# Kernel tuning notes

Measured on AMD Instinct MI355X. Metric: run time of the kernel, lower is better.

## Reference

```python
import jax, jax.numpy as jnp
import numpy as np

N_NODES = 100000
N_EDGES = 1600000
D_IN = 128
D_HID = 128
D_OUT = 128
N_LAYERS = 4


def setup_inputs() -> dict:
    key = jax.random.key(0)
    ks = jax.random.split(key, 8)
    x = jax.random.normal(ks[0], (N_NODES, D_IN), dtype=jnp.float32)
    edge_index = jax.random.randint(ks[1], (2, N_EDGES), 0, N_NODES, dtype=jnp.int64)
    s = 1.0 / np.sqrt(D_IN)
    # All layers are 128->128, so stack weights: [L, in, out]
    W_lin = jax.random.uniform(ks[2], (N_LAYERS, D_IN, D_HID), minval=-s, maxval=s, dtype=jnp.float32)
    W_film = jax.random.uniform(ks[3], (N_LAYERS, D_IN, 2 * D_HID), minval=-s, maxval=s, dtype=jnp.float32)
    b_film = jax.random.uniform(ks[4], (N_LAYERS, 2 * D_HID), minval=-s, maxval=s, dtype=jnp.float32)
    W_skip = jax.random.uniform(ks[5], (N_LAYERS, D_IN, D_HID), minval=-s, maxval=s, dtype=jnp.float32)
    W_fskip = jax.random.uniform(ks[6], (N_LAYERS, D_IN, 2 * D_HID), minval=-s, maxval=s, dtype=jnp.float32)
    return {"x": x, "edge_index": edge_index, "W_lin": W_lin, "W_film": W_film,
            "b_film": b_film, "W_skip": W_skip, "W_fskip": W_fskip}


def _film_conv(x, src, dst, deg_inv, W_l, W_f, b_f, W_s, W_fs, c):
    # skip path: FiLM-modulated self transform
    bg_s = x @ W_fs                       # [N, 2C], no bias
    beta_s, gamma_s = bg_s[:, :c], bg_s[:, c:]
    out = jax.nn.relu(gamma_s * (x @ W_s) + beta_s)
    # message path: FiLM params from target node, features from source node
    bg = x @ W_f + b_f                    # [N, 2C]
    beta, gamma = bg[:, :c], bg[:, c:]
    h = x @ W_l                           # [N, C]
    msg = jax.nn.relu(gamma[dst] * h[src] + beta[dst])  # [E, C]
    agg = jax.ops.segment_sum(msg, dst, num_segments=x.shape[0]) * deg_inv  # mean aggr
    return out + agg


def reference(x, edge_index, W_lin, W_film, b_film, W_skip, W_fskip):
    src, dst = edge_index[0], edge_index[1]
    n = x.shape[0]
    deg = jax.ops.segment_sum(jnp.ones((src.shape[0],), x.dtype), dst, num_segments=n)
    deg_inv = (1.0 / jnp.maximum(deg, 1.0))[:, None]   # clamp(min=1) like PyG mean
    for l in range(N_LAYERS):
        x = _film_conv(x, src, dst, deg_inv, W_lin[l], W_film[l], b_film[l],
                       W_skip[l], W_fskip[l], D_HID)
        if l < N_LAYERS - 1:
            x = jax.nn.relu(x)
    return x
```

## Files before the change

### kernel.cpp

```cpp
#include <hip/hip_runtime.h>
#include <hip/hip_bf16.h>

#define N_NODES 100000
#define N_PAD   100096
#define N_EDGES 1600000
#define NXCD    8
#define NRANGE  ((N_NODES + NXCD - 1) / NXCD)
#define NSLICE  256

typedef __bf16 bf16x8 __attribute__((ext_vector_type(8)));
typedef float  f32x4  __attribute__((ext_vector_type(4)));

__device__ __forceinline__ void gload16(const void* g, void* s) {
    __builtin_amdgcn_global_load_lds(
        (const __attribute__((address_space(1))) unsigned int*)g,
        (__attribute__((address_space(3))) unsigned int*)s, 16, 0, 0);
}

__device__ __forceinline__ float2 bf2f(unsigned p) {
    float2 r;
    union { unsigned u; float f; } a, b;
    a.u = p << 16;
    b.u = p & 0xffff0000u;
    r.x = a.f; r.y = b.f;
    return r;
}
__device__ __forceinline__ unsigned f2bf2(float x, float y) {
    unsigned lo = (unsigned)__builtin_bit_cast(unsigned short, __float2bfloat16(x));
    unsigned hi = (unsigned)__builtin_bit_cast(unsigned short, __float2bfloat16(y));
    return lo | (hi << 16);
}

__global__ void detect_kernel(const unsigned* __restrict__ e, int* __restrict__ flag) {
    __shared__ int nz;
    if (threadIdx.x == 0) nz = 0;
    __syncthreads();
    int local = 0;
    for (int i = threadIdx.x; i < 1024; i += blockDim.x)
        if (e[2 * i + 1] != 0) local = 1;
    if (local) atomicOr(&nz, 1);
    __syncthreads();
    if (threadIdx.x == 0) *flag = (nz == 0) ? 1 : 0;
}

__device__ __forceinline__ int edge_at(const unsigned* __restrict__ e, long idx, int is64) {
    return (int)(is64 ? e[2 * idx] : e[idx]);
}

__global__ void hist_kernel(const unsigned* __restrict__ e, const int* __restrict__ flag,
                            int* __restrict__ counts) {
    int i = blockIdx.x * blockDim.x + threadIdx.x;
    if (i >= N_EDGES) return;
    int is64 = *flag;
    int d = edge_at(e, (long)N_EDGES + i, is64);
    atomicAdd(&counts[d], 1);
}

__global__ void scan1_kernel(const int* __restrict__ counts, int* __restrict__ blockSums) {
    __shared__ int red[256];
    int base = blockIdx.x * 1024;
    int sum = 0;
    for (int i = threadIdx.x; i < 1024; i += 256) {
        int idx = base + i;
        sum += (idx < N_NODES) ? counts[idx] : 0;
    }
    red[threadIdx.x] = sum;
    __syncthreads();
    for (int s = 128; s > 0; s >>= 1) {
        if (threadIdx.x < s) red[threadIdx.x] += red[threadIdx.x + s];
        __syncthreads();
    }
    if (threadIdx.x == 0) blockSums[blockIdx.x] = red[0];
}

__global__ void scan2_kernel(int* __restrict__ blockSums, int nb, int* __restrict__ row_ptr) {
    int run = 0;
    for (int i = 0; i < nb; ++i) { int v = blockSums[i]; blockSums[i] = run; run += v; }
    row_ptr[N_NODES] = run;
}

__global__ void scan3_kernel(const int* __restrict__ counts, const int* __restrict__ blockSums,
                             int* __restrict__ row_ptr, int* __restrict__ cursor,
                             float* __restrict__ deg_inv) {
    __shared__ int lds[256];
    int base = blockIdx.x * 1024;
    int t = threadIdx.x;
    int v[4];
    int s = 0;
    for (int i = 0; i < 4; ++i) {
        int idx = base + t * 4 + i;
        v[i] = (idx < N_NODES) ? counts[idx] : 0;
        s += v[i];
    }
    lds[t] = s;
    __syncthreads();
    for (int off = 1; off < 256; off <<= 1) {
        int add = (t >= off) ? lds[t - off] : 0;
        __syncthreads();
        lds[t] += add;
        __syncthreads();
    }
    int excl = lds[t] - s + blockSums[blockIdx.x];
    for (int i = 0; i < 4; ++i) {
        int idx = base + t * 4 + i;
        if (idx < N_NODES) {
            row_ptr[idx] = excl;
            cursor[idx]  = excl;
            deg_inv[idx] = 1.0f / fmaxf((float)v[i], 1.0f);
            excl += v[i];
        }
    }
}

__global__ __launch_bounds__(256) void fill2_kernel(
    const unsigned* __restrict__ e, const int* __restrict__ flag,
    int* __restrict__ cursor, int* __restrict__ csr_src) {
    const int r     = blockIdx.x & (NXCD - 1);
    const int slice = blockIdx.x >> 3;
    const int lo = r * NRANGE;
    const int hi = min(lo + NRANGE, N_NODES);
    const int is64 = *flag;
    const int per = (N_EDGES + NSLICE - 1) / NSLICE;
    const int i0 = slice * per;
    const int i1 = min(i0 + per, N_EDGES);
    for (int i = i0 + (int)threadIdx.x; i < i1; i += 256) {
        int d = edge_at(e, (long)N_EDGES + i, is64);
        if (d >= lo && d < hi) {
            int s = edge_at(e, (long)i, is64);
            int pos = atomicAdd(&cursor[d], 1);
            csr_src[pos] = s;
        }
    }
}

__global__ void bt_prep_kernel(const float* __restrict__ Wl, const float* __restrict__ Wf,
                               const float* __restrict__ Ws, const float* __restrict__ Wfs,
                               __hip_bfloat16* __restrict__ Bt) {
    int idx = blockIdx.x * 256 + threadIdx.x;
    if (idx >= 4 * 768 * 128) return;
    int k   = idx % 128;
    int row = (idx / 128) % 768;
    int lay = idx / (128 * 768);
    float w;
    if (row < 128) {
        w = Wl[(size_t)lay * 16384 + k * 128 + row];
    } else if (row < 384) {
        w = Wf[(size_t)lay * 32768 + k * 256 + (row - 128)];
    } else {
        int rr = row - 384;
        int g = rr >> 4, within = rr & 15;
        int kind = g % 3;
        int c = (g / 3) * 16 + within;
        if (kind == 0)      w = Ws [(size_t)lay * 16384 + k * 128 + c];
        else if (kind == 1) w = Wfs[(size_t)lay * 32768 + k * 256 + c];
        else                w = Wfs[(size_t)lay * 32768 + k * 256 + 128 + c];
    }
    Bt[idx] = __float2bfloat16(w);
}

__global__ void cast_kernel(const float* __restrict__ x, unsigned* __restrict__ A2) {
    long i = (long)blockIdx.x * 256 + threadIdx.x;
    if (i >= (long)N_NODES * 64) return;
    float2 v = ((const float2*)x)[i];
    A2[i] = f2bf2(v.x, v.y);
}

__global__ __launch_bounds__(256, 2) void mfma_gemm_kernel(
    const __hip_bfloat16* __restrict__ A,
    const __hip_bfloat16* __restrict__ Bt,
    const float* __restrict__ bfilm,
    __hip_bfloat16* __restrict__ hbuf,
    __hip_bfloat16* __restrict__ bgbuf)
{
    __shared__ alignas(16) unsigned char lds_raw[32768];
    unsigned char* ldsA = lds_raw;
    unsigned char* ldsB = lds_raw + 16384;

    const int t  = threadIdx.x;
    const int mt = blockIdx.x / 3;
    const int jt = blockIdx.x % 3;
    const long node0 = (long)mt * 128;
    const int w  = t >> 6, l = t & 63;
    const int wm = w >> 1, wn = w & 1;
    const int lr = l & 15;
    const int kq16 = (l >> 4) << 4;
    const int sw = (lr & 7) << 4;

    const int sr  = t >> 3;
    const int scb = (t & 7) << 4;
    const int scbs = scb ^ ((sr & 7) << 4);

    const char* Abase = (const char*)A;
    const char* Bbase = (const char*)Bt + (size_t)(jt * 128) * 256;

    f32x4 acc[4][4];
    #pragma unroll
    for (int mi = 0; mi < 4; ++mi)
        #pragma unroll
        for (int ni = 0; ni < 4; ++ni)
            #pragma unroll
            for (int j = 0; j < 4; ++j) acc[mi][ni][j] = 0.f;

    #pragma unroll
    for (int ks = 0; ks < 2; ++ks) {
        const int k0 = ks * 64;
        #pragma unroll
        for (int i = 0; i < 4; ++i) {
            const int r = (i << 5) + sr;
            gload16(Abase + (node0 + r) * 256 + (size_t)k0 * 2 + scbs,
                    ldsA + (((i << 8) + t) << 4));
            gload16(Bbase + (size_t)r * 256 + (size_t)k0 * 2 + scbs,
                    ldsB + (((i << 8) + t) << 4));
        }
        __syncthreads();

        #pragma unroll
        for (int kh = 0; kh < 2; ++kh) {
            const int kbs = ((kh << 6) + kq16) ^ sw;
            bf16x8 af[4], bfr[4];
            #pragma unroll
            for (int mi = 0; mi < 4; ++mi)
                af[mi] = *(const bf16x8*)(ldsA + (wm * 64 + mi * 16 + lr) * 128 + kbs);
            #pragma unroll
            for (int ni = 0; ni < 4; ++ni)
                bfr[ni] = *(const bf16x8*)(ldsB + (wn * 64 + ni * 16 + lr) * 128 + kbs);
            #pragma unroll
            for (int mi = 0; mi < 4; ++mi)
                #pragma unroll
                for (int ni = 0; ni < 4; ++ni)
                    acc[mi][ni] = __builtin_amdgcn_mfma_f32_16x16x32_bf16(
                        af[mi], bfr[ni], acc[mi][ni], 0, 0, 0);
        }
        __syncthreads();
    }

    const int col = lr;
    const int rb  = (l >> 4) << 2;
    if (jt == 0) {
        #pragma unroll
        for (int mi = 0; mi < 4; ++mi)
            #pragma unroll
            for (int ni = 0; ni < 4; ++ni) {
                const int n = wn * 64 + ni * 16 + col;
                #pragma unroll
                for (int j = 0; j < 4; ++j) {
                    long node = node0 + wm * 64 + mi * 16 + rb + j;
                    if (node < N_NODES)
                        hbuf[node * 128 + n] = __float2bfloat16(acc[mi][ni][j]);
                }
            }
    } else {
        const int c0 = (jt - 1) * 128;
        #pragma unroll
        for (int mi = 0; mi < 4; ++mi)
            #pragma unroll
            for (int ni = 0; ni < 4; ++ni) {
                const int n = wn * 64 + ni * 16 + col;
                const float bb = bfilm[c0 + n];
                #pragma unroll
                for (int j = 0; j < 4; ++j) {
                    long node = node0 + wm * 64 + mi * 16 + rb + j;
                    if (node < N_NODES)
                        bgbuf[node * 256 + c0 + n] = __float2bfloat16(acc[mi][ni][j] + bb);
                }
            }
    }
}

__global__ __launch_bounds__(256, 2) void skip_gemm_kernel(
    const __hip_bfloat16* __restrict__ A,
    const __hip_bfloat16* __restrict__ Bs,
    float* __restrict__ skb)
{
    __shared__ alignas(16) unsigned char lds_raw[16384 + 12288];
    unsigned char* ldsA = lds_raw;
    unsigned char* ldsB = lds_raw + 16384;

    const int t  = threadIdx.x;
    const int mt = blockIdx.x >> 2;
    const int jt2 = blockIdx.x & 3;
    const long node0 = (long)mt * 128;
    const int w  = t >> 6, l = t & 63;
    const int wm = w >> 1, wn = w & 1;
    const int lr = l & 15;
    const int kq16 = (l >> 4) << 4;
    const int sw = (lr & 7) << 4;

    const int sr  = t >> 3;
    const int scb = (t & 7) << 4;
    const int scbs = scb ^ ((sr & 7) << 4);

    const char* Abase = (const char*)A;
    const char* Bbase = (const char*)Bs + (size_t)(jt2 * 96) * 256;

    f32x4 acc[4][3];
    #pragma unroll
    for (int mi = 0; mi < 4; ++mi)
        #pragma unroll
        for (int ni = 0; ni < 3; ++ni)
            #pragma unroll
            for (int j = 0; j < 4; ++j) acc[mi][ni][j] = 0.f;

    #pragma unroll
    for (int ks = 0; ks < 2; ++ks) {
        const int k0 = ks * 64;
        #pragma unroll
        for (int i = 0; i < 4; ++i) {
            const int r = (i << 5) + sr;
            gload16(Abase + (node0 + r) * 256 + (size_t)k0 * 2 + scbs,
                    ldsA + (((i << 8) + t) << 4));
        }
        #pragma unroll
        for (int i = 0; i < 3; ++i) {
            const int r = (i << 5) + sr;
            gload16(Bbase + (size_t)r * 256 + (size_t)k0 * 2 + scbs,
                    ldsB + (((i << 8) + t) << 4));
        }
        __syncthreads();

        #pragma unroll
        for (int kh = 0; kh < 2; ++kh) {
            const int kbs = ((kh << 6) + kq16) ^ sw;
            bf16x8 af[4], bfr[3];
            #pragma unroll
            for (int mi = 0; mi < 4; ++mi)
                af[mi] = *(const bf16x8*)(ldsA + (wm * 64 + mi * 16 + lr) * 128 + kbs);
            #pragma unroll
            for (int ni = 0; ni < 3; ++ni)
                bfr[ni] = *(const bf16x8*)(ldsB + (wn * 48 + ni * 16 + lr) * 128 + kbs);
            #pragma unroll
            for (int mi = 0; mi < 4; ++mi)
                #pragma unroll
                for (int ni = 0; ni < 3; ++ni)
                    acc[mi][ni] = __builtin_amdgcn_mfma_f32_16x16x32_bf16(
                        af[mi], bfr[ni], acc[mi][ni], 0, 0, 0);
        }
        __syncthreads();
    }

    const int c  = (2 * jt2 + wn) * 16 + lr;
    const int rb = (l >> 4) << 2;
    #pragma unroll
    for (int mi = 0; mi < 4; ++mi)
        #pragma unroll
        for (int j = 0; j < 4; ++j) {
            long node = node0 + wm * 64 + mi * 16 + rb + j;
            if (node < N_NODES) {
                float o = fmaxf(acc[mi][2][j] * acc[mi][0][j] + acc[mi][1][j], 0.f);
                skb[node * 128 + c] = o;
            }
        }
}

__global__ __launch_bounds__(256) void agg_kernel(
    const unsigned* __restrict__ h2,
    const unsigned* __restrict__ bg2,
    const int* __restrict__ row_ptr, const int* __restrict__ csr_src,
    const float* __restrict__ deg_inv,
    const float* __restrict__ skb,
    unsigned* __restrict__ Anext2,
    float* __restrict__ fout)
{
    const int t = threadIdx.x;
    const int v = blockIdx.x * 4 + (t >> 6);
    const int l = t & 63;

    const float2 beta  = bf2f(bg2[(size_t)v * 128 + l]);
    const float2 gamma = bf2f(bg2[(size_t)v * 128 + 64 + l]);
    const float2 sk = *(const float2*)(skb + (size_t)v * 128 + 2 * l);
    const float dinv = deg_inv[v];

    const int b = row_ptr[v];
    const int e = row_ptr[v + 1];

    float2 a0 = {0.f, 0.f}, a1 = {0.f, 0.f}, a2 = {0.f, 0.f}, a3 = {0.f, 0.f};
    int i = b;
    for (; i + 4 <= e; i += 4) {
        const int s0 = csr_src[i];
        const int s1 = csr_src[i + 1];
        const int s2 = csr_src[i + 2];
        const int s3 = csr_src[i + 3];
        const unsigned p0 = h2[(size_t)s0 * 64 + l];
        const unsigned p1 = h2[(size_t)s1 * 64 + l];
        const unsigned p2 = h2[(size_t)s2 * 64 + l];
        const unsigned p3 = h2[(size_t)s3 * 64 + l];
        float2 h0 = bf2f(p0), h1 = bf2f(p1), h2f = bf2f(p2), h3 = bf2f(p3);
        a0.x += fmaxf(gamma.x * h0.x + beta.x, 0.f);
        a0.y += fmaxf(gamma.y * h0.y + beta.y, 0.f);
        a1.x += fmaxf(gamma.x * h1.x + beta.x, 0.f);
        a1.y += fmaxf(gamma.y * h1.y + beta.y, 0.f);
        a2.x += fmaxf(gamma.x * h2f.x + beta.x, 0.f);
        a2.y += fmaxf(gamma.y * h2f.y + beta.y, 0.f);
        a3.x += fmaxf(gamma.x * h3.x + beta.x, 0.f);
        a3.y += fmaxf(gamma.y * h3.y + beta.y, 0.f);
    }
    for (; i < e; ++i) {
        const int s0 = csr_src[i];
        float2 h0 = bf2f(h2[(size_t)s0 * 64 + l]);
        a0.x += fmaxf(gamma.x * h0.x + beta.x, 0.f);
        a0.y += fmaxf(gamma.y * h0.y + beta.y, 0.f);
    }
    float2 acc;
    acc.x = (a0.x + a1.x) + (a2.x + a3.x);
    acc.y = (a0.y + a1.y) + (a2.y + a3.y);

    float o0 = sk.x + acc.x * dinv;
    float o1 = sk.y + acc.y * dinv;

    if (Anext2) {
        Anext2[(size_t)v * 64 + l] = f2bf2(o0, o1);
    } else {
        *(float2*)(fout + (size_t)v * 128 + 2 * l) = make_float2(o0, o1);
    }
}

extern "C" void kernel_launch(void* const* d_in, const int* in_sizes, int n_in,
                              void* d_out, int out_size, void* d_ws, size_t ws_size,
                              hipStream_t stream) {
    const float*    x_in    = (const float*)d_in[0];
    const unsigned* eidx    = (const unsigned*)d_in[1];
    const float*    W_lin   = (const float*)d_in[2];
    const float*    W_film  = (const float*)d_in[3];
    const float*    b_film  = (const float*)d_in[4];
    const float*    W_skip  = (const float*)d_in[5];
    const float*    W_fskip = (const float*)d_in[6];
    float*          out     = (float*)d_out;

    char* ws = (char*)d_ws;
    size_t off = 0;
    auto alloc = [&](size_t bytes) -> void* {
        void* p = ws + off;
        off = (off + bytes + 255) & ~(size_t)255;
        return p;
    };
    int*   flag      = (int*)alloc(4);
    int*   counts    = (int*)alloc((size_t)N_NODES * 4);
    int*   row_ptr   = (int*)alloc((size_t)(N_NODES + 1) * 4);
    int*   cursor    = (int*)alloc((size_t)N_NODES * 4);
    int*   blockSums = (int*)alloc(128 * 4);
    float* deg_inv   = (float*)alloc((size_t)N_NODES * 4);
    int*   csr_src   = (int*)alloc((size_t)N_EDGES * 4);
    __hip_bfloat16* Abuf  = (__hip_bfloat16*)alloc((size_t)N_PAD * 128 * 2);
    __hip_bfloat16* BtAll = (__hip_bfloat16*)alloc((size_t)4 * 768 * 128 * 2);
    __hip_bfloat16* hbuf  = (__hip_bfloat16*)alloc((size_t)N_NODES * 128 * 2);
    __hip_bfloat16* bgbuf = (__hip_bfloat16*)alloc((size_t)N_NODES * 256 * 2);
    float* skb = out;
    (void)ws_size; (void)in_sizes; (void)n_in; (void)out_size;

    const int NB_SCAN = (N_NODES + 1023) / 1024;
    const int EB = (N_EDGES + 255) / 256;

    hipMemsetAsync(counts, 0, (size_t)N_NODES * 4, stream);
    detect_kernel<<<1, 256, 0, stream>>>(eidx, flag);
    hist_kernel<<<EB, 256, 0, stream>>>(eidx, flag, counts);
    scan1_kernel<<<NB_SCAN, 256, 0, stream>>>(counts, blockSums);
    scan2_kernel<<<1, 1, 0, stream>>>(blockSums, NB_SCAN, row_ptr);
    scan3_kernel<<<NB_SCAN, 256, 0, stream>>>(counts, blockSums, row_ptr, cursor, deg_inv);
    fill2_kernel<<<NXCD * NSLICE, 256, 0, stream>>>(eidx, flag, cursor, csr_src);

    cast_kernel<<<(N_NODES * 64 + 255) / 256, 256, 0, stream>>>(x_in, (unsigned*)Abuf);
    bt_prep_kernel<<<(4 * 768 * 128 + 255) / 256, 256, 0, stream>>>(
        W_lin, W_film, W_skip, W_fskip, BtAll);

    const int MT = N_PAD / 128;
    const int AGG_B = (N_NODES + 3) / 4;
    for (int l = 0; l < 4; ++l) {
        const __hip_bfloat16* Bt_l = BtAll + (size_t)l * 768 * 128;
        mfma_gemm_kernel<<<MT * 3, 256, 0, stream>>>(
            Abuf, Bt_l, b_film + (size_t)l * 256, hbuf, bgbuf);
        skip_gemm_kernel<<<MT * 4, 256, 0, stream>>>(
            Abuf, Bt_l + (size_t)384 * 128, skb);
        agg_kernel<<<AGG_B, 256, 0, stream>>>(
            (const unsigned*)hbuf, (const unsigned*)bgbuf,
            row_ptr, csr_src, deg_inv, skb,
            (l < 3) ? (unsigned*)Abuf : (unsigned*)nullptr,
            (l == 3) ? out : (float*)nullptr);
    }
}
```

Measured before the change: 713.5 us.

## Fuse skip and message GEMMs, store skip in bf16, split edges across half-waves

Merges the message GEMM and the skip GEMM into one launch with 7 column tiles per row tile, which removes one kernel launch per layer. The skip output now goes to a separate bf16 buffer instead of fp32 in the output, halving that write and its later read. The aggregation kernel has each half-wavefront handle alternate edges with 8-byte loads covering 4 channels, then combines the halves with a cross-lane shuffle. This raises gather parallelism per node, at the cost of lower skip-path precision and an extra shuffle reduction.

```diff
diff --git a/kernel.cpp b/kernel.cpp
--- a/kernel.cpp
+++ b/kernel.cpp
@@ -165,20 +165,21 @@
     A2[i] = f2bf2(v.x, v.y);
 }
 
-__global__ __launch_bounds__(256, 2) void mfma_gemm_kernel(
+__global__ __launch_bounds__(256, 2) void fused_gemm_kernel(
     const __hip_bfloat16* __restrict__ A,
     const __hip_bfloat16* __restrict__ Bt,
     const float* __restrict__ bfilm,
     __hip_bfloat16* __restrict__ hbuf,
-    __hip_bfloat16* __restrict__ bgbuf)
+    __hip_bfloat16* __restrict__ bgbuf,
+    __hip_bfloat16* __restrict__ skbh)
 {
     __shared__ alignas(16) unsigned char lds_raw[32768];
     unsigned char* ldsA = lds_raw;
     unsigned char* ldsB = lds_raw + 16384;
 
     const int t  = threadIdx.x;
-    const int mt = blockIdx.x / 3;
-    const int jt = blockIdx.x % 3;
+    const int mt = blockIdx.x / 7;
+    const int jt = blockIdx.x % 7;
     const long node0 = (long)mt * 128;
     const int w  = t >> 6, l = t & 63;
     const int wm = w >> 1, wn = w & 1;
@@ -191,226 +192,229 @@
     const int scbs = scb ^ ((sr & 7) << 4);
 
     const char* Abase = (const char*)A;
-    const char* Bbase = (const char*)Bt + (size_t)(jt * 128) * 256;
-
-    f32x4 acc[4][4];
-    #pragma unroll
-    for (int mi = 0; mi < 4; ++mi)
-        #pragma unroll
-        for (int ni = 0; ni < 4; ++ni)
-            #pragma unroll
-            for (int j = 0; j < 4; ++j) acc[mi][ni][j] = 0.f;
-
-    #pragma unroll
-    for (int ks = 0; ks < 2; ++ks) {
-        const int k0 = ks * 64;
-        #pragma unroll
-        for (int i = 0; i < 4; ++i) {
-            const int r = (i << 5) + sr;
-            gload16(Abase + (node0 + r) * 256 + (size_t)k0 * 2 + scbs,
-                    ldsA + (((i << 8) + t) << 4));
-            gload16(Bbase + (size_t)r * 256 + (size_t)k0 * 2 + scbs,
-                    ldsB + (((i << 8) + t) << 4));
-        }
-        __syncthreads();
-
-        #pragma unroll
-        for (int kh = 0; kh < 2; ++kh) {
-            const int kbs = ((kh << 6) + kq16) ^ sw;
-            bf16x8 af[4], bfr[4];
-            #pragma unroll
-            for (int mi = 0; mi < 4; ++mi)
-                af[mi] = *(const bf16x8*)(ldsA + (wm * 64 + mi * 16 + lr) * 128 + kbs);
-            #pragma unroll
-            for (int ni = 0; ni < 4; ++ni)
-                bfr[ni] = *(const bf16x8*)(ldsB + (wn * 64 + ni * 16 + lr) * 128 + kbs);
-            #pragma unroll
-            for (int mi = 0; mi < 4; ++mi)
-                #pragma unroll
-                for (int ni = 0; ni < 4; ++ni)
-                    acc[mi][ni] = __builtin_amdgcn_mfma_f32_16x16x32_bf16(
-                        af[mi], bfr[ni], acc[mi][ni], 0, 0, 0);
-        }
-        __syncthreads();
-    }
-
-    const int col = lr;
-    const int rb  = (l >> 4) << 2;
-    if (jt == 0) {
+
+    if (jt < 3) {
+        const char* Bbase = (const char*)Bt + (size_t)(jt * 128) * 256;
+        f32x4 acc[4][4];
         #pragma unroll
         for (int mi = 0; mi < 4; ++mi)
             #pragma unroll
-            for (int ni = 0; ni < 4; ++ni) {
-                const int n = wn * 64 + ni * 16 + col;
-                #pragma unroll
-                for (int j = 0; j < 4; ++j) {
-                    long node = node0 + wm * 64 + mi * 16 + rb + j;
-                    if (node < N_NODES)
-                        hbuf[node * 128 + n] = __float2bfloat16(acc[mi][ni][j]);
+            for (int ni = 0; ni < 4; ++ni)
+                #pragma unroll
+                for (int j = 0; j < 4; ++j) acc[mi][ni][j] = 0.f;
+
+        #pragma unroll
+        for (int ks = 0; ks < 2; ++ks) {
+            const int k0 = ks * 64;
+            #pragma unroll
+            for (int i = 0; i < 4; ++i) {
+                const int r = (i << 5) + sr;
+                gload16(Abase + (node0 + r) * 256 + (size_t)k0 * 2 + scbs,
+                        ldsA + (((i << 8) + t) << 4));
+                gload16(Bbase + (size_t)r * 256 + (size_t)k0 * 2 + scbs,
+                        ldsB + (((i << 8) + t) << 4));
+            }
+            __syncthreads();
+
+            #pragma unroll
+            for (int kh = 0; kh < 2; ++kh) {
+                const int kbs = ((kh << 6) + kq16) ^ sw;
+                bf16x8 af[4], bfr[4];
+                #pragma unroll
+                for (int mi = 0; mi < 4; ++mi)
+                    af[mi] = *(const bf16x8*)(ldsA + (wm * 64 + mi * 16 + lr) * 128 + kbs);
+                #pragma unroll
+                for (int ni = 0; ni < 4; ++ni)
+                    bfr[ni] = *(const bf16x8*)(ldsB + (wn * 64 + ni * 16 + lr) * 128 + kbs);
+                #pragma unroll
+                for (int mi = 0; mi < 4; ++mi)
+                    #pragma unroll
+                    for (int ni = 0; ni < 4; ++ni)
+                        acc[mi][ni] = __builtin_amdgcn_mfma_f32_16x16x32_bf16(
+                            af[mi], bfr[ni], acc[mi][ni], 0, 0, 0);
+            }
+            __syncthreads();
+        }
+
+        const int col = lr;
+        const int rb  = (l >> 4) << 2;
+        if (jt == 0) {
+            #pragma unroll
+            for (int mi = 0; mi < 4; ++mi)
+                #pragma unroll
+                for (int ni = 0; ni < 4; ++ni) {
+                    const int n = wn * 64 + ni * 16 + col;
+                    #pragma unroll
+                    for (int j = 0; j < 4; ++j) {
+                        long node = node0 + wm * 64 + mi * 16 + rb + j;
+                        if (node < N_NODES)
+                            hbuf[node * 128 + n] = __float2bfloat16(acc[mi][ni][j]);
+                    }
                 }
-            }
+        } else {
+            const int c0 = (jt - 1) * 128;
+            #pragma unroll
+            for (int mi = 0; mi < 4; ++mi)
+                #pragma unroll
+                for (int ni = 0; ni < 4; ++ni) {
+                    const int n = wn * 64 + ni * 16 + col;
+                    const float bb = bfilm[c0 + n];
+                    #pragma unroll
+                    for (int j = 0; j < 4; ++j) {
+                        long node = node0 + wm * 64 + mi * 16 + rb + j;
+                        if (node < N_NODES)
+                            bgbuf[node * 256 + c0 + n] = __float2bfloat16(acc[mi][ni][j] + bb);
+                    }
+                }
+        }
     } else {
-        const int c0 = (jt - 1) * 128;
+        const int jt2 = jt - 3;
+        const char* Bbase = (const char*)Bt + (size_t)(384 + jt2 * 96) * 256;
+        f32x4 acc[4][3];
         #pragma unroll
         for (int mi = 0; mi < 4; ++mi)
             #pragma unroll
-            for (int ni = 0; ni < 4; ++ni) {
-                const int n = wn * 64 + ni * 16 + col;
-                const float bb = bfilm[c0 + n];
-                #pragma unroll
-                for (int j = 0; j < 4; ++j) {
-                    long node = node0 + wm * 64 + mi * 16 + rb + j;
-                    if (node < N_NODES)
-                        bgbuf[node * 256 + c0 + n] = __float2bfloat16(acc[mi][ni][j] + bb);
+            for (int ni = 0; ni < 3; ++ni)
+                #pragma unroll
+                for (int j = 0; j < 4; ++j) acc[mi][ni][j] = 0.f;
+
+        #pragma unroll
+        for (int ks = 0; ks < 2; ++ks) {
+            const int k0 = ks * 64;
+            #pragma unroll
+            for (int i = 0; i < 4; ++i) {
+                const int r = (i << 5) + sr;
+                gload16(Abase + (node0 + r) * 256 + (size_t)k0 * 2 + scbs,
+                        ldsA + (((i << 8) + t) << 4));
+            }
+            #pragma unroll
+            for (int i = 0; i < 3; ++i) {
+                const int r = (i << 5) + sr;
+                gload16(Bbase + (size_t)r * 256 + (size_t)k0 * 2 + scbs,
+                        ldsB + (((i << 8) + t) << 4));
+            }
+            __syncthreads();
+
+            #pragma unroll
+            for (int kh = 0; kh < 2; ++kh) {
+                const int kbs = ((kh << 6) + kq16) ^ sw;
+                bf16x8 af[4], bfr[3];
+                #pragma unroll
+                for (int mi = 0; mi < 4; ++mi)
+                    af[mi] = *(const bf16x8*)(ldsA + (wm * 64 + mi * 16 + lr) * 128 + kbs);
+                #pragma unroll
+                for (int ni = 0; ni < 3; ++ni)
+                    bfr[ni] = *(const bf16x8*)(ldsB + (wn * 48 + ni * 16 + lr) * 128 + kbs);
+                #pragma unroll
+                for (int mi = 0; mi < 4; ++mi)
+                    #pragma unroll
+                    for (int ni = 0; ni < 3; ++ni)
+                        acc[mi][ni] = __builtin_amdgcn_mfma_f32_16x16x32_bf16(
+                            af[mi], bfr[ni], acc[mi][ni], 0, 0, 0);
+            }
+            __syncthreads();
+        }
+
+        const int c  = (2 * jt2 + wn) * 16 + lr;
+        const int rb = (l >> 4) << 2;
+        #pragma unroll
+        for (int mi = 0; mi < 4; ++mi)
+            #pragma unroll
+            for (int j = 0; j < 4; ++j) {
+                long node = node0 + wm * 64 + mi * 16 + rb + j;
+                if (node < N_NODES) {
+                    float o = fmaxf(acc[mi][2][j] * acc[mi][0][j] + acc[mi][1][j], 0.f);
+                    skbh[node * 128 + c] = __float2bfloat16(o);
                 }
             }
     }
 }
 
-__global__ __launch_bounds__(256, 2) void skip_gemm_kernel(
-    const __hip_bfloat16* __restrict__ A,
-    const __hip_bfloat16* __restrict__ Bs,
-    float* __restrict__ skb)
-{
-    __shared__ alignas(16) unsigned char lds_raw[16384 + 12288];
-    unsigned char* ldsA = lds_raw;
-    unsigned char* ldsB = lds_raw + 16384;
-
-    const int t  = threadIdx.x;
-    const int mt = blockIdx.x >> 2;
-    const int jt2 = blockIdx.x & 3;
-    const long node0 = (long)mt * 128;
-    const int w  = t >> 6, l = t & 63;
-    const int wm = w >> 1, wn = w & 1;
-    const int lr = l & 15;
-    const int kq16 = (l >> 4) << 4;
-    const int sw = (lr & 7) << 4;
-
-    const int sr  = t >> 3;
-    const int scb = (t & 7) << 4;
-    const int scbs = scb ^ ((sr & 7) << 4);
-
-    const char* Abase = (const char*)A;
-    const char* Bbase = (const char*)Bs + (size_t)(jt2 * 96) * 256;
-
-    f32x4 acc[4][3];
-    #pragma unroll
-    for (int mi = 0; mi < 4; ++mi)
-        #pragma unroll
-        for (int ni = 0; ni < 3; ++ni)
-            #pragma unroll
-            for (int j = 0; j < 4; ++j) acc[mi][ni][j] = 0.f;
-
-    #pragma unroll
-    for (int ks = 0; ks < 2; ++ks) {
-        const int k0 = ks * 64;
-        #pragma unroll
-        for (int i = 0; i < 4; ++i) {
-            const int r = (i << 5) + sr;
-            gload16(Abase + (node0 + r) * 256 + (size_t)k0 * 2 + scbs,
-                    ldsA + (((i << 8) + t) << 4));
-        }
-        #pragma unroll
-        for (int i = 0; i < 3; ++i) {
-            const int r = (i << 5) + sr;
-            gload16(Bbase + (size_t)r * 256 + (size_t)k0 * 2 + scbs,
-                    ldsB + (((i << 8) + t) << 4));
-        }
-        __syncthreads();
-
-        #pragma unroll
-        for (int kh = 0; kh < 2; ++kh) {
-            const int kbs = ((kh << 6) + kq16) ^ sw;
-            bf16x8 af[4], bfr[3];
-            #pragma unroll
-            for (int mi = 0; mi < 4; ++mi)
-                af[mi] = *(const bf16x8*)(ldsA + (wm * 64 + mi * 16 + lr) * 128 + kbs);
-            #pragma unroll
-            for (int ni = 0; ni < 3; ++ni)
-                bfr[ni] = *(const bf16x8*)(ldsB + (wn * 48 + ni * 16 + lr) * 128 + kbs);
-            #pragma unroll
-            for (int mi = 0; mi < 4; ++mi)
-                #pragma unroll
-                for (int ni = 0; ni < 3; ++ni)
-                    acc[mi][ni] = __builtin_amdgcn_mfma_f32_16x16x32_bf16(
-                        af[mi], bfr[ni], acc[mi][ni], 0, 0, 0);
-        }
-        __syncthreads();
-    }
-
-    const int c  = (2 * jt2 + wn) * 16 + lr;
-    const int rb = (l >> 4) << 2;
-    #pragma unroll
-    for (int mi = 0; mi < 4; ++mi)
-        #pragma unroll
-        for (int j = 0; j < 4; ++j) {
-            long node = node0 + wm * 64 + mi * 16 + rb + j;
-            if (node < N_NODES) {
-                float o = fmaxf(acc[mi][2][j] * acc[mi][0][j] + acc[mi][1][j], 0.f);
-                skb[node * 128 + c] = o;
-            }
-        }
-}
-
 __global__ __launch_bounds__(256) void agg_kernel(
-    const unsigned* __restrict__ h2,
-    const unsigned* __restrict__ bg2,
+    const uint2* __restrict__ h22,
+    const uint2* __restrict__ bgu2,
     const int* __restrict__ row_ptr, const int* __restrict__ csr_src,
     const float* __restrict__ deg_inv,
-    const float* __restrict__ skb,
-    unsigned* __restrict__ Anext2,
-    float* __restrict__ fout)
+    const uint2* __restrict__ sku2,
+    uint2* __restrict__ An2,
+    float4* __restrict__ fo4)
 {
     const int t = threadIdx.x;
     const int v = blockIdx.x * 4 + (t >> 6);
     const int l = t & 63;
-
-    const float2 beta  = bf2f(bg2[(size_t)v * 128 + l]);
-    const float2 gamma = bf2f(bg2[(size_t)v * 128 + 64 + l]);
-    const float2 sk = *(const float2*)(skb + (size_t)v * 128 + 2 * l);
+    const int half = l >> 5;
+    const unsigned c = l & 31;
+
+    const uint2 bu = bgu2[(size_t)v * 64 + c];
+    const uint2 gu = bgu2[(size_t)v * 64 + 32 + c];
+    const float2 be01 = bf2f(bu.x), be23 = bf2f(bu.y);
+    const float2 ga01 = bf2f(gu.x), ga23 = bf2f(gu.y);
     const float dinv = deg_inv[v];
 
     const int b = row_ptr[v];
     const int e = row_ptr[v + 1];
-
-    float2 a0 = {0.f, 0.f}, a1 = {0.f, 0.f}, a2 = {0.f, 0.f}, a3 = {0.f, 0.f};
-    int i = b;
-    for (; i + 4 <= e; i += 4) {
-        const int s0 = csr_src[i];
-        const int s1 = csr_src[i + 1];
-        const int s2 = csr_src[i + 2];
-        const int s3 = csr_src[i + 3];
-        const unsigned p0 = h2[(size_t)s0 * 64 + l];
-        const unsigned p1 = h2[(size_t)s1 * 64 + l];
-        const unsigned p2 = h2[(size_t)s2 * 64 + l];
-        const unsigned p3 = h2[(size_t)s3 * 64 + l];
-        float2 h0 = bf2f(p0), h1 = bf2f(p1), h2f = bf2f(p2), h3 = bf2f(p3);
-        a0.x += fmaxf(gamma.x * h0.x + beta.x, 0.f);
-        a0.y += fmaxf(gamma.y * h0.y + beta.y, 0.f);
-        a1.x += fmaxf(gamma.x * h1.x + beta.x, 0.f);
-        a1.y += fmaxf(gamma.y * h1.y + beta.y, 0.f);
-        a2.x += fmaxf(gamma.x * h2f.x + beta.x, 0.f);
-        a2.y += fmaxf(gamma.y * h2f.y + beta.y, 0.f);
-        a3.x += fmaxf(gamma.x * h3.x + beta.x, 0.f);
-        a3.y += fmaxf(gamma.y * h3.y + beta.y, 0.f);
-    }
-    for (; i < e; ++i) {
-        const int s0 = csr_src[i];
-        float2 h0 = bf2f(h2[(size_t)s0 * 64 + l]);
-        a0.x += fmaxf(gamma.x * h0.x + beta.x, 0.f);
-        a0.y += fmaxf(gamma.y * h0.y + beta.y, 0.f);
-    }
-    float2 acc;
-    acc.x = (a0.x + a1.x) + (a2.x + a3.x);
-    acc.y = (a0.y + a1.y) + (a2.y + a3.y);
-
-    float o0 = sk.x + acc.x * dinv;
-    float o1 = sk.y + acc.y * dinv;
-
-    if (Anext2) {
-        Anext2[(size_t)v * 64 + l] = f2bf2(o0, o1);
-    } else {
-        *(float2*)(fout + (size_t)v * 128 + 2 * l) = make_float2(o0, o1);
+    const int ne = e - b;
+    const int npair = ne >> 1;
+
+    f32x4 ac0 = {0,0,0,0}, ac1 = {0,0,0,0}, ac2 = {0,0,0,0}, ac3 = {0,0,0,0};
+
+    const int* cp = csr_src + b + half;
+
+#define ACC(A_, P_) do {                                   \
+        float2 h01 = bf2f((P_).x), h23 = bf2f((P_).y);     \
+        (A_)[0] += fmaxf(ga01.x * h01.x + be01.x, 0.f);    \
+        (A_)[1] += fmaxf(ga01.y * h01.y + be01.y, 0.f);    \
+        (A_)[2] += fmaxf(ga23.x * h23.x + be23.x, 0.f);    \
+        (A_)[3] += fmaxf(ga23.y * h23.y + be23.y, 0.f);    \
+    } while (0)
+
+    int pi = 0;
+    for (; pi + 4 <= npair; pi += 4) {
+        const int i0 = 2 * pi;
+        const unsigned s0 = (unsigned)cp[i0];
+        const unsigned s1 = (unsigned)cp[i0 + 2];
+        const unsigned s2 = (unsigned)cp[i0 + 4];
+        const unsigned s3 = (unsigned)cp[i0 + 6];
+        const uint2 p0 = h22[s0 * 32u + c];
+        const uint2 p1 = h22[s1 * 32u + c];
+        const uint2 p2 = h22[s2 * 32u + c];
+        const uint2 p3 = h22[s3 * 32u + c];
+        ACC(ac0, p0); ACC(ac1, p1); ACC(ac2, p2); ACC(ac3, p3);
+    }
+    for (; pi < npair; ++pi) {
+        const unsigned s0 = (unsigned)cp[2 * pi];
+        const uint2 p0 = h22[s0 * 32u + c];
+        ACC(ac0, p0);
+    }
+    if ((ne & 1) && half == 0) {
+        const unsigned s0 = (unsigned)csr_src[e - 1];
+        const uint2 p0 = h22[s0 * 32u + c];
+        ACC(ac1, p0);
+    }
+#undef ACC
+
+    float r0 = (ac0[0] + ac1[0]) + (ac2[0] + ac3[0]);
+    float r1 = (ac0[1] + ac1[1]) + (ac2[1] + ac3[1]);
+    float r2 = (ac0[2] + ac1[2]) + (ac2[2] + ac3[2]);
+    float r3 = (ac0[3] + ac1[3]) + (ac2[3] + ac3[3]);
+    r0 += __shfl_xor(r0, 32);
+    r1 += __shfl_xor(r1, 32);
+    r2 += __shfl_xor(r2, 32);
+    r3 += __shfl_xor(r3, 32);
+
+    const uint2 sk = sku2[(size_t)v * 32 + c];
+    const float2 s01 = bf2f(sk.x), s23 = bf2f(sk.y);
+    const float o0 = s01.x + r0 * dinv;
+    const float o1 = s01.y + r1 * dinv;
+    const float o2 = s23.x + r2 * dinv;
+    const float o3 = s23.y + r3 * dinv;
+
+    if (half == 0) {
+        if (An2) {
+            An2[(size_t)v * 32 + c] = make_uint2(f2bf2(o0, o1), f2bf2(o2, o3));
+        } else {
+            fo4[(size_t)v * 32 + c] = make_float4(o0, o1, o2, o3);
+        }
     }
 }
 
@@ -444,7 +448,7 @@
     __hip_bfloat16* BtAll = (__hip_bfloat16*)alloc((size_t)4 * 768 * 128 * 2);
     __hip_bfloat16* hbuf  = (__hip_bfloat16*)alloc((size_t)N_NODES * 128 * 2);
     __hip_bfloat16* bgbuf = (__hip_bfloat16*)alloc((size_t)N_NODES * 256 * 2);
-    float* skb = out;
+    __hip_bfloat16* skbh  = (__hip_bfloat16*)alloc((size_t)N_NODES * 128 * 2);
     (void)ws_size; (void)in_sizes; (void)n_in; (void)out_size;
 
     const int NB_SCAN = (N_NODES + 1023) / 1024;
@@ -463,17 +467,15 @@
         W_lin, W_film, W_skip, W_fskip, BtAll);
 
     const int MT = N_PAD / 128;
-    const int AGG_B = (N_NODES + 3) / 4;
+    const int AGG_B = N_NODES / 4;
     for (int l = 0; l < 4; ++l) {
         const __hip_bfloat16* Bt_l = BtAll + (size_t)l * 768 * 128;
-        mfma_gemm_kernel<<<MT * 3, 256, 0, stream>>>(
-            Abuf, Bt_l, b_film + (size_t)l * 256, hbuf, bgbuf);
-        skip_gemm_kernel<<<MT * 4, 256, 0, stream>>>(
-            Abuf, Bt_l + (size_t)384 * 128, skb);
+        fused_gemm_kernel<<<MT * 7, 256, 0, stream>>>(
+            Abuf, Bt_l, b_film + (size_t)l * 256, hbuf, bgbuf, skbh);
         agg_kernel<<<AGG_B, 256, 0, stream>>>(
-            (const unsigned*)hbuf, (const unsigned*)bgbuf,
-            row_ptr, csr_src, deg_inv, skb,
-            (l < 3) ? (unsigned*)Abuf : (unsigned*)nullptr,
-            (l == 3) ? out : (float*)nullptr);
-    }
-}
+            (const uint2*)hbuf, (const uint2*)bgbuf,
+            row_ptr, csr_src, deg_inv, (const uint2*)skbh,
+            (l < 3) ? (uint2*)Abuf : (uint2*)nullptr,
+            (l == 3) ? (float4*)out : (float4*)nullptr);
+    }
+}
```

Result: faster. 659.2 us (-7.6%).
